# Performance work log

Hardware: AMD Instinct MI355X
Metric: run time of the kernel (lower is better)

The kernel has to match this reference:

```python
import jax, jax.numpy as jnp
import numpy as np

EPS = 1e-6
N_HEADS = 16
KV_HEADS = 4
HEAD_DIM = 64
N_REP = N_HEADS // KV_HEADS
N_EXPERTS = 8
TOP_K = 2


def _rms_norm(x, w):
    return x * jax.lax.rsqrt(jnp.mean(x * x, axis=-1, keepdims=True) + EPS) * w


def _apply_rope(x, fc):
    # x: (B,T,H,D); fc: (T, D//2, 2) holding (cos, sin)
    B, T, H, D = x.shape
    xr = x.reshape(B, T, H, D // 2, 2)
    f = fc.reshape(1, T, 1, D // 2, 2)
    re = xr[..., 0] * f[..., 0] - xr[..., 1] * f[..., 1]
    im = xr[..., 1] * f[..., 0] + xr[..., 0] * f[..., 1]
    return jnp.stack([re, im], axis=-1).reshape(B, T, H, D)


def _silu(x):
    return x * jax.nn.sigmoid(x)


def setup_inputs():
    key = jax.random.key(0)
    ks = jax.random.split(key, 16)
    B, T, C = 4, 1024, 1024
    IE, IS = 1024, 2048  # expert_inter_dim, shared inter_dim
    s = 0.02
    x = jax.random.normal(ks[0], (B, T, C), jnp.float32)
    inv_freq = 1.0 / (10000.0 ** (np.arange(0, HEAD_DIM, 2, dtype=np.float32) / HEAD_DIM))
    ang = np.outer(np.arange(T, dtype=np.float32), inv_freq)
    freq_cis = jnp.asarray(np.stack([np.cos(ang), np.sin(ang)], axis=-1), jnp.float32)
    causal = np.tril(np.ones((T, T), dtype=bool))
    mask = jnp.asarray(np.where(causal, 0.0, -1e9), dtype=jnp.float32).reshape(1, 1, T, T)
    window = jnp.zeros((1, 1, T, T), jnp.float32)
    return {
        "x": x,
        "freq_cis": freq_cis,
        "mask": mask,
        "window": window,
        "norm1_w": jnp.ones((C,), jnp.float32),
        "wq": jax.random.normal(ks[1], (N_HEADS * HEAD_DIM, C), jnp.float32) * s,
        "wk": jax.random.normal(ks[2], (KV_HEADS * HEAD_DIM, C), jnp.float32) * s,
        "wv": jax.random.normal(ks[3], (KV_HEADS * HEAD_DIM, C), jnp.float32) * s,
        "wo": jax.random.normal(ks[4], (C, N_HEADS * HEAD_DIM), jnp.float32) * s,
        "norm2_w": jnp.ones((C,), jnp.float32),
        "gate_w": jax.random.normal(ks[5], (N_EXPERTS, C), jnp.float32) * s,
        "exp_w1": jax.random.normal(ks[6], (N_EXPERTS, IE, C), jnp.float32) * s,
        "exp_w2": jax.random.normal(ks[7], (N_EXPERTS, IE, C), jnp.float32) * s,
        "exp_wp": jax.random.normal(ks[8], (N_EXPERTS, C, IE), jnp.float32) * s,
        "sh_w1": jax.random.normal(ks[9], (IS, C), jnp.float32) * s,
        "sh_w2": jax.random.normal(ks[10], (IS, C), jnp.float32) * s,
        "sh_wp": jax.random.normal(ks[11], (C, IS), jnp.float32) * s,
        "start_pos": 0,
    }


def reference(x, freq_cis, mask, window, norm1_w, wq, wk, wv, wo, norm2_w,
              gate_w, exp_w1, exp_w2, exp_wp, sh_w1, sh_w2, sh_wp, start_pos):
    B, T, C = x.shape
    # ---- pre-norm attention (GQA, Global mask, eval: no dropout) ----
    xn = _rms_norm(x, norm1_w)
    q = (xn @ wq.T).reshape(B, T, N_HEADS, HEAD_DIM)
    k = (xn @ wk.T).reshape(B, T, KV_HEADS, HEAD_DIM)
    v = (xn @ wv.T).reshape(B, T, KV_HEADS, HEAD_DIM)
    q = _apply_rope(q, freq_cis)
    k = _apply_rope(k, freq_cis)
    k = jnp.repeat(k, N_REP, axis=2)  # (B,T,H,D)
    v = jnp.repeat(v, N_REP, axis=2)
    scale = 1.0 / np.sqrt(HEAD_DIM).astype(np.float32)
    att = jnp.einsum("bqhd,bkhd->bhqk", q, k) * scale + mask
    p = jax.nn.softmax(att, axis=-1)
    o = jnp.einsum("bhqk,bkhd->bqhd", p, v).reshape(B, T, C)
    x = x + o @ wo.T
    # ---- pre-norm MoE FFN ----
    xn2 = _rms_norm(x, norm2_w).reshape(-1, C)  # (N,C)
    scores = xn2 @ gate_w.T                      # gate logits, returned
    probs = jax.nn.softmax(scores, axis=-1)
    top_w, top_i = jax.lax.top_k(probs, TOP_K)   # (N,K)
    # dense combine weights (N,E): zero for non-selected experts
    wfull = jnp.sum(jax.nn.one_hot(top_i, N_EXPERTS, dtype=x.dtype) * top_w[..., None], axis=1)
    h = _silu(jnp.einsum("nc,eic->eni", xn2, exp_w1)) * jnp.einsum("nc,eic->eni", xn2, exp_w2)
    ye = jnp.einsum("eni,eci->enc", h, exp_wp)   # per-expert outputs
    y = jnp.einsum("ne,enc->nc", wfull, ye)      # routed combine
    z = (_silu(xn2 @ sh_w1.T) * (xn2 @ sh_w2.T)) @ sh_wp.T  # shared expert
    out = x + (y + z).reshape(B, T, C)
    return out, scores
```

## Files before the change

### kernel.cpp

```cpp
#include <hip/hip_runtime.h>


typedef __bf16 bf16_t;
typedef __bf16 bf16x8 __attribute__((ext_vector_type(8)));
typedef __bf16 bf16x4 __attribute__((ext_vector_type(4)));
typedef float  f32x4  __attribute__((ext_vector_type(4)));

#define LQKV 1536

#define GLD16(gp, lp) __builtin_amdgcn_global_load_lds(                         \
    (const __attribute__((address_space(1))) void*)(gp),                        \
    (__attribute__((address_space(3))) void*)(lp), 16, 0, 0)

#define PIPE_BARRIER() do {                                                     \
    asm volatile("s_waitcnt vmcnt(0)" ::: "memory");                            \
    __builtin_amdgcn_s_barrier();                                               \
} while (0)

__global__ __launch_bounds__(256) void convert_k(
    const float* __restrict__ src, bf16_t* __restrict__ dst)
{
    size_t i = (size_t)blockIdx.x * 256 + threadIdx.x;
    float4 v = *((const float4*)src + i);
    bf16x4 o;
    o[0] = (bf16_t)v.x; o[1] = (bf16_t)v.y; o[2] = (bf16_t)v.z; o[3] = (bf16_t)v.w;
    *((bf16x4*)dst + i) = o;
}

struct Cvt8 {
    const float* s[8];
    bf16_t* d[8];
    int cum[9];
    int nseg;
};

__global__ __launch_bounds__(256) void convert_multi_k(Cvt8 j)
{
    int blk = blockIdx.x;
    int seg = 0;
    while (seg + 1 < j.nseg && blk >= j.cum[seg + 1]) ++seg;
    size_t i = (size_t)(blk - j.cum[seg]) * 256 + threadIdx.x;
    float4 v = *((const float4*)j.s[seg] + i);
    bf16x4 o;
    o[0] = (bf16_t)v.x; o[1] = (bf16_t)v.y; o[2] = (bf16_t)v.z; o[3] = (bf16_t)v.w;
    *((bf16x4*)j.d[seg] + i) = o;
}

__global__ __launch_bounds__(256) void gemm_bt(
    const bf16_t* __restrict__ A, const bf16_t* __restrict__ W,
    int M, int N, int K, int ldw, int mode,
    float* __restrict__ outF, bf16_t* __restrict__ outB,
    const float* __restrict__ resF, float* __restrict__ outF2)
{
    __shared__ __align__(16) bf16_t sA[2][128 * 64];
    __shared__ __align__(16) bf16_t sB[2][128 * 64];
    const int tid  = threadIdx.x;
    const int bm   = blockIdx.y * 128, bn = blockIdx.x * 128;
    const int lane = tid & 63;
    const int wv   = tid >> 6;
    const int wm   = (wv >> 1) * 64, wn = (wv & 1) * 64;
    const int lr   = lane & 15;
    const int kg   = lane >> 4;
    const int swz  = (lr & 7) << 3;

    f32x4 acc[4][4];
    #pragma unroll
    for (int i = 0; i < 4; ++i)
        #pragma unroll
        for (int j = 0; j < 4; ++j)
            acc[i][j] = f32x4{0.f, 0.f, 0.f, 0.f};

    auto STAGE = [&](int b, int k0) {
        #pragma unroll
        for (int p = 0; p < 4; ++p) {
            int idx = p * 256 + tid;
            int row = idx >> 3;
            int ch  = ((idx & 7) * 8) ^ ((row & 7) << 3);
            GLD16(A + (size_t)(bm + row) * K   + k0 + ch, sA[b] + idx * 8);
            GLD16(W + (size_t)(bn + row) * ldw + k0 + ch, sB[b] + idx * 8);
        }
    };

    STAGE(0, 0);
    PIPE_BARRIER();
    int cur = 0;
    for (int k0 = 0; k0 < K; k0 += 64) {
        if (k0 + 64 < K) STAGE(cur ^ 1, k0 + 64);
        #pragma unroll
        for (int ks = 0; ks < 2; ++ks) {
            bf16x8 af[4], bfr[4];
            #pragma unroll
            for (int i = 0; i < 4; ++i)
                af[i] = *(const bf16x8*)(sA[cur] + (wm + i * 16 + lr) * 64 +
                                         ((ks * 32 + kg * 8) ^ swz));
            #pragma unroll
            for (int j = 0; j < 4; ++j)
                bfr[j] = *(const bf16x8*)(sB[cur] + (wn + j * 16 + lr) * 64 +
                                          ((ks * 32 + kg * 8) ^ swz));
            #pragma unroll
            for (int i = 0; i < 4; ++i)
                #pragma unroll
                for (int j = 0; j < 4; ++j)
                    acc[i][j] = __builtin_amdgcn_mfma_f32_16x16x32_bf16(
                        af[i], bfr[j], acc[i][j], 0, 0, 0);
        }
        PIPE_BARRIER();
        cur ^= 1;
    }

    #pragma unroll
    for (int i = 0; i < 4; ++i) {
        #pragma unroll
        for (int j = 0; j < 4; ++j) {
            #pragma unroll
            for (int rr = 0; rr < 4; ++rr) {
                int m = bm + wm + i * 16 + kg * 4 + rr;
                int n = bn + wn + j * 16 + lr;
                size_t o = (size_t)m * N + n;
                float v = acc[i][j][rr];
                if (mode == 0)      outF[o] = v;
                else if (mode == 1) outB[o] = (bf16_t)v;
                else if (mode == 2) {
                    float r = v + resF[o];
                    outF[o] = r;
                    if (outF2) outF2[o] = r;
                } else              outF[o] += v;
            }
        }
    }
}

__global__ __launch_bounds__(256) void gemm_glu(
    const bf16_t* __restrict__ A, const bf16_t* __restrict__ W1,
    const bf16_t* __restrict__ W2, int M, int N, int K,
    bf16_t* __restrict__ out)
{
    __shared__ __align__(16) bf16_t sA[2][128 * 32];
    __shared__ __align__(16) bf16_t sB1[2][128 * 32];
    __shared__ __align__(16) bf16_t sB2[2][128 * 32];
    const int tid  = threadIdx.x;
    const int bm   = blockIdx.y * 128, bn = blockIdx.x * 128;
    const int lane = tid & 63;
    const int wv   = tid >> 6;
    const int wm   = (wv >> 1) * 64, wn = (wv & 1) * 64;
    const int lr   = lane & 15;
    const int kg   = lane >> 4;
    const int rsw  = (lr >> 1) & 3;

    f32x4 acc1[4][4], acc2[4][4];
    #pragma unroll
    for (int i = 0; i < 4; ++i)
        #pragma unroll
        for (int j = 0; j < 4; ++j) {
            acc1[i][j] = f32x4{0.f, 0.f, 0.f, 0.f};
            acc2[i][j] = f32x4{0.f, 0.f, 0.f, 0.f};
        }

    auto STAGE = [&](int b, int k0) {
        #pragma unroll
        for (int p = 0; p < 2; ++p) {
            int idx = p * 256 + tid;
            int row = idx >> 2;
            int ch  = 8 * ((idx & 3) ^ ((idx >> 3) & 3));
            GLD16(A  + (size_t)(bm + row) * K + k0 + ch, sA[b]  + idx * 8);
            GLD16(W1 + (size_t)(bn + row) * K + k0 + ch, sB1[b] + idx * 8);
            GLD16(W2 + (size_t)(bn + row) * K + k0 + ch, sB2[b] + idx * 8);
        }
    };

    STAGE(0, 0);
    PIPE_BARRIER();
    int cur = 0;
    for (int k0 = 0; k0 < K; k0 += 32) {
        if (k0 + 32 < K) STAGE(cur ^ 1, k0 + 32);
        bf16x8 af[4], b1[4], b2[4];
        #pragma unroll
        for (int i = 0; i < 4; ++i)
            af[i] = *(const bf16x8*)(sA[cur] + (wm + i * 16 + lr) * 32 +
                                     8 * (kg ^ rsw));
        #pragma unroll
        for (int j = 0; j < 4; ++j) {
            b1[j] = *(const bf16x8*)(sB1[cur] + (wn + j * 16 + lr) * 32 +
                                     8 * (kg ^ rsw));
            b2[j] = *(const bf16x8*)(sB2[cur] + (wn + j * 16 + lr) * 32 +
                                     8 * (kg ^ rsw));
        }
        #pragma unroll
        for (int i = 0; i < 4; ++i)
            #pragma unroll
            for (int j = 0; j < 4; ++j) {
                acc1[i][j] = __builtin_amdgcn_mfma_f32_16x16x32_bf16(
                    af[i], b1[j], acc1[i][j], 0, 0, 0);
                acc2[i][j] = __builtin_amdgcn_mfma_f32_16x16x32_bf16(
                    af[i], b2[j], acc2[i][j], 0, 0, 0);
            }
        PIPE_BARRIER();
        cur ^= 1;
    }

    #pragma unroll
    for (int i = 0; i < 4; ++i) {
        #pragma unroll
        for (int j = 0; j < 4; ++j) {
            #pragma unroll
            for (int rr = 0; rr < 4; ++rr) {
                int m = bm + wm + i * 16 + kg * 4 + rr;
                int n = bn + wn + j * 16 + lr;
                float v1 = acc1[i][j][rr], v2 = acc2[i][j][rr];
                out[(size_t)m * N + n] = (bf16_t)(v1 / (1.f + __expf(-v1)) * v2);
            }
        }
    }
}

__device__ __forceinline__ int seg_off(const int* cnt, int e)
{
    int r = 0;
    #pragma unroll
    for (int k = 0; k < 8; ++k) if (k < e) r += (cnt[k] + 127) & ~127;
    return r;
}

__global__ __launch_bounds__(256) void glu_gather(
    const bf16_t* __restrict__ A, const bf16_t* __restrict__ W1,
    const bf16_t* __restrict__ W2, const int* __restrict__ tok_list,
    const int* __restrict__ cnt, bf16_t* __restrict__ h)
{
    const int e = blockIdx.y >> 5, t = blockIdx.y & 31;
    const int ce = cnt[e];
    if (t * 128 >= ce) return;
    const int hbase = seg_off(cnt, e) + t * 128;
    const bf16_t* W1e = W1 + (size_t)e * 1048576;
    const bf16_t* W2e = W2 + (size_t)e * 1048576;

    __shared__ __align__(16) bf16_t sA[2][128 * 32];
    __shared__ __align__(16) bf16_t sB1[2][128 * 32];
    __shared__ __align__(16) bf16_t sB2[2][128 * 32];
    const int tid  = threadIdx.x;
    const int bn   = blockIdx.x * 128;
    const int lane = tid & 63;
    const int wv   = tid >> 6;
    const int wm   = (wv >> 1) * 64, wn = (wv & 1) * 64;
    const int lr   = lane & 15;
    const int kg   = lane >> 4;
    const int rsw  = (lr >> 1) & 3;

    int tok2[2];
    #pragma unroll
    for (int p = 0; p < 2; ++p)
        tok2[p] = tok_list[e * 4096 + t * 128 + ((p * 256 + tid) >> 2)];

    f32x4 acc1[4][4], acc2[4][4];
    #pragma unroll
    for (int i = 0; i < 4; ++i)
        #pragma unroll
        for (int j = 0; j < 4; ++j) {
            acc1[i][j] = f32x4{0.f, 0.f, 0.f, 0.f};
            acc2[i][j] = f32x4{0.f, 0.f, 0.f, 0.f};
        }

    auto STAGE = [&](int b, int k0) {
        #pragma unroll
        for (int p = 0; p < 2; ++p) {
            int idx = p * 256 + tid;
            int row = idx >> 2;
            int ch  = 8 * ((idx & 3) ^ ((idx >> 3) & 3));
            GLD16(A   + (size_t)tok2[p] * 1024 + k0 + ch,    sA[b]  + idx * 8);
            GLD16(W1e + (size_t)(bn + row) * 1024 + k0 + ch, sB1[b] + idx * 8);
            GLD16(W2e + (size_t)(bn + row) * 1024 + k0 + ch, sB2[b] + idx * 8);
        }
    };

    STAGE(0, 0);
    PIPE_BARRIER();
    int cur = 0;
    for (int k0 = 0; k0 < 1024; k0 += 32) {
        if (k0 + 32 < 1024) STAGE(cur ^ 1, k0 + 32);
        bf16x8 af[4], b1[4], b2[4];
        #pragma unroll
        for (int i = 0; i < 4; ++i)
            af[i] = *(const bf16x8*)(sA[cur] + (wm + i * 16 + lr) * 32 +
                                     8 * (kg ^ rsw));
        #pragma unroll
        for (int j = 0; j < 4; ++j) {
            b1[j] = *(const bf16x8*)(sB1[cur] + (wn + j * 16 + lr) * 32 +
                                     8 * (kg ^ rsw));
            b2[j] = *(const bf16x8*)(sB2[cur] + (wn + j * 16 + lr) * 32 +
                                     8 * (kg ^ rsw));
        }
        #pragma unroll
        for (int i = 0; i < 4; ++i)
            #pragma unroll
            for (int j = 0; j < 4; ++j) {
                acc1[i][j] = __builtin_amdgcn_mfma_f32_16x16x32_bf16(
                    af[i], b1[j], acc1[i][j], 0, 0, 0);
                acc2[i][j] = __builtin_amdgcn_mfma_f32_16x16x32_bf16(
                    af[i], b2[j], acc2[i][j], 0, 0, 0);
            }
        PIPE_BARRIER();
        cur ^= 1;
    }

    #pragma unroll
    for (int i = 0; i < 4; ++i) {
        #pragma unroll
        for (int j = 0; j < 4; ++j) {
            #pragma unroll
            for (int rr = 0; rr < 4; ++rr) {
                int rl = wm + i * 16 + kg * 4 + rr;
                int n  = bn + wn + j * 16 + lr;
                float v1 = acc1[i][j][rr], v2 = acc2[i][j][rr];
                h[(size_t)(hbase + rl) * 1024 + n] =
                    (bf16_t)(v1 / (1.f + __expf(-v1)) * v2);
            }
        }
    }
}

__global__ __launch_bounds__(256) void down_gather(
    const bf16_t* __restrict__ h, const bf16_t* __restrict__ Wp,
    const int* __restrict__ tok_list, const float* __restrict__ w_list,
    const int* __restrict__ cnt, float* __restrict__ out)
{
    const int e = blockIdx.y >> 5, t = blockIdx.y & 31;
    const int ce = cnt[e];
    if (t * 128 >= ce) return;
    const int hbase = seg_off(cnt, e) + t * 128;
    const bf16_t* We = Wp + (size_t)e * 1048576;

    __shared__ __align__(16) bf16_t sA[2][128 * 64];
    __shared__ __align__(16) bf16_t sB[2][128 * 64];
    const int tid  = threadIdx.x;
    const int bn   = blockIdx.x * 128;
    const int lane = tid & 63;
    const int wv   = tid >> 6;
    const int wm   = (wv >> 1) * 64, wn = (wv & 1) * 64;
    const int lr   = lane & 15;
    const int kg   = lane >> 4;
    const int swz  = (lr & 7) << 3;

    f32x4 acc[4][4];
    #pragma unroll
    for (int i = 0; i < 4; ++i)
        #pragma unroll
        for (int j = 0; j < 4; ++j)
            acc[i][j] = f32x4{0.f, 0.f, 0.f, 0.f};

    auto STAGE = [&](int b, int k0) {
        #pragma unroll
        for (int p = 0; p < 4; ++p) {
            int idx = p * 256 + tid;
            int row = idx >> 3;
            int ch  = ((idx & 7) * 8) ^ ((row & 7) << 3);
            GLD16(h  + (size_t)(hbase + row) * 1024 + k0 + ch, sA[b] + idx * 8);
            GLD16(We + (size_t)(bn + row) * 1024 + k0 + ch,    sB[b] + idx * 8);
        }
    };

    STAGE(0, 0);
    PIPE_BARRIER();
    int cur = 0;
    for (int k0 = 0; k0 < 1024; k0 += 64) {
        if (k0 + 64 < 1024) STAGE(cur ^ 1, k0 + 64);
        #pragma unroll
        for (int ks = 0; ks < 2; ++ks) {
            bf16x8 af[4], bfr[4];
            #pragma unroll
            for (int i = 0; i < 4; ++i)
                af[i] = *(const bf16x8*)(sA[cur] + (wm + i * 16 + lr) * 64 +
                                         ((ks * 32 + kg * 8) ^ swz));
            #pragma unroll
            for (int j = 0; j < 4; ++j)
                bfr[j] = *(const bf16x8*)(sB[cur] + (wn + j * 16 + lr) * 64 +
                                          ((ks * 32 + kg * 8) ^ swz));
            #pragma unroll
            for (int i = 0; i < 4; ++i)
                #pragma unroll
                for (int j = 0; j < 4; ++j)
                    acc[i][j] = __builtin_amdgcn_mfma_f32_16x16x32_bf16(
                        af[i], bfr[j], acc[i][j], 0, 0, 0);
        }
        PIPE_BARRIER();
        cur ^= 1;
    }

    #pragma unroll
    for (int i = 0; i < 4; ++i) {
        #pragma unroll
        for (int rr = 0; rr < 4; ++rr) {
            int g = t * 128 + wm + i * 16 + kg * 4 + rr;
            if (g < ce) {
                int   tok = tok_list[e * 4096 + g];
                float wgt = w_list[e * 4096 + g];
                #pragma unroll
                for (int j = 0; j < 4; ++j) {
                    int n = bn + wn + j * 16 + lr;
                    atomicAdd(&out[(size_t)tok * 1024 + n], wgt * acc[i][j][rr]);
                }
            }
        }
    }
}

__global__ __launch_bounds__(256) void rmsnorm_k(
    const float* __restrict__ src, const float* __restrict__ w,
    bf16_t* __restrict__ dst)
{
    const int row = blockIdx.x, tid = threadIdx.x;
    float4 t4 = *((const float4*)src + (size_t)row * 256 + tid);
    float ssum = t4.x*t4.x + t4.y*t4.y + t4.z*t4.z + t4.w*t4.w;
    #pragma unroll
    for (int off = 32; off > 0; off >>= 1) ssum += __shfl_down(ssum, off);
    __shared__ float red[4];
    if ((tid & 63) == 0) red[tid >> 6] = ssum;
    __syncthreads();
    float total = red[0] + red[1] + red[2] + red[3];
    float rms = rsqrtf(total * (1.0f / 1024.0f) + 1e-6f);
    float4 w4 = *((const float4*)w + tid);
    bf16x4 o4;
    o4[0] = (bf16_t)(t4.x * rms * w4.x);
    o4[1] = (bf16_t)(t4.y * rms * w4.y);
    o4[2] = (bf16_t)(t4.z * rms * w4.z);
    o4[3] = (bf16_t)(t4.w * rms * w4.w);
    *((bf16x4*)dst + (size_t)row * 256 + tid) = o4;
}

__global__ __launch_bounds__(256) void rmsnorm_gate_k(
    const float* __restrict__ src, const float* __restrict__ w,
    const float* __restrict__ gw, bf16_t* __restrict__ dst,
    float* __restrict__ scores, int* __restrict__ topi,
    float* __restrict__ topw)
{
    const int row = blockIdx.x, tid = threadIdx.x;
    float4 t4 = *((const float4*)src + (size_t)row * 256 + tid);
    float ssum = t4.x*t4.x + t4.y*t4.y + t4.z*t4.z + t4.w*t4.w;
    #pragma unroll
    for (int off = 32; off > 0; off >>= 1) ssum += __shfl_down(ssum, off);
    __shared__ float red[4];
    if ((tid & 63) == 0) red[tid >> 6] = ssum;
    __syncthreads();
    float total = red[0] + red[1] + red[2] + red[3];
    float rms = rsqrtf(total * (1.0f / 1024.0f) + 1e-6f);
    float4 w4 = *((const float4*)w + tid);
    float4 f4;
    f4.x = t4.x * rms * w4.x;
    f4.y = t4.y * rms * w4.y;
    f4.z = t4.z * rms * w4.z;
    f4.w = t4.w * rms * w4.w;
    bf16x4 o4;
    o4[0] = (bf16_t)f4.x; o4[1] = (bf16_t)f4.y;
    o4[2] = (bf16_t)f4.z; o4[3] = (bf16_t)f4.w;
    *((bf16x4*)dst + (size_t)row * 256 + tid) = o4;

    float a[8];
    #pragma unroll
    for (int e = 0; e < 8; ++e) {
        float4 g4 = *((const float4*)(gw + (size_t)e * 1024) + tid);
        a[e] = f4.x * g4.x + f4.y * g4.y + f4.z * g4.z + f4.w * g4.w;
    }
    #pragma unroll
    for (int e = 0; e < 8; ++e)
        #pragma unroll
        for (int off = 32; off > 0; off >>= 1) a[e] += __shfl_down(a[e], off);
    __shared__ float gred[4][8];
    if ((tid & 63) == 0)
        #pragma unroll
        for (int e = 0; e < 8; ++e) gred[tid >> 6][e] = a[e];
    __syncthreads();
    if (tid == 0) {
        float lg[8];
        #pragma unroll
        for (int e = 0; e < 8; ++e)
            lg[e] = gred[0][e] + gred[1][e] + gred[2][e] + gred[3][e];
        #pragma unroll
        for (int e = 0; e < 8; ++e) scores[(size_t)row * 8 + e] = lg[e];
        float mx = lg[0];
        #pragma unroll
        for (int e = 1; e < 8; ++e) mx = fmaxf(mx, lg[e]);
        float p[8], sum = 0.f;
        #pragma unroll
        for (int e = 0; e < 8; ++e) { p[e] = __expf(lg[e] - mx); sum += p[e]; }
        float inv = 1.0f / sum;
        #pragma unroll
        for (int e = 0; e < 8; ++e) p[e] *= inv;
        int i1 = 0;
        #pragma unroll
        for (int e = 1; e < 8; ++e) if (p[e] > p[i1]) i1 = e;
        int i2 = (i1 == 0) ? 1 : 0;
        #pragma unroll
        for (int e = 0; e < 8; ++e) if (e != i1 && p[e] > p[i2]) i2 = e;
        topi[row] = i1 | (i2 << 8);
        topw[row * 2]     = p[i1];
        topw[row * 2 + 1] = p[i2];
    }
}

__global__ __launch_bounds__(256) void build_lists_k(
    const int* __restrict__ topi, const float* __restrict__ topw,
    int* __restrict__ tok_list, float* __restrict__ w_list,
    int* __restrict__ cnt)
{
    const int e = blockIdx.x;
    const int tid = threadIdx.x, lane = tid & 63, wv = tid >> 6;
    __shared__ int wc[4];
    int base = 0;
    for (int t0 = 0; t0 < 4096; t0 += 256) {
        int tok = t0 + tid;
        int ti = topi[tok];
        int i1 = ti & 255, i2 = (ti >> 8) & 255;
        bool m = (i1 == e) || (i2 == e);
        unsigned long long b = __ballot(m);
        if (lane == 0) wc[wv] = __popcll(b);
        __syncthreads();
        int pos = base;
        #pragma unroll
        for (int k = 0; k < 4; ++k) if (k < wv) pos += wc[k];
        pos += __popcll(b & ((1ull << lane) - 1ull));
        if (m) {
            tok_list[e * 4096 + pos] = tok;
            w_list[e * 4096 + pos]   = (i1 == e) ? topw[tok * 2] : topw[tok * 2 + 1];
        }
        base += wc[0] + wc[1] + wc[2] + wc[3];
        __syncthreads();
    }
    int padded = (base + 127) & ~127;
    for (int p = base + tid; p < padded; p += 256) tok_list[e * 4096 + p] = 0;
    if (tid == 0) cnt[e] = base;
}

__global__ __launch_bounds__(256) void rope_all_k(
    bf16_t* __restrict__ qkv, const float* __restrict__ fc)
{
    int idx = blockIdx.x * 256 + threadIdx.x;
    int pr = idx & 31;
    int hn = idx >> 5;
    int h  = hn % 20;
    int n  = hn / 20;
    int tpos = n & 1023;
    const float* f = fc + ((size_t)tpos * 32 + pr) * 2;
    float c = f[0], s = f[1];
    int col = (h < 16) ? h * 64 : 1024 + (h - 16) * 64;
    size_t base = (size_t)n * LQKV + col + pr * 2;
    float x0 = (float)qkv[base], x1 = (float)qkv[base + 1];
    qkv[base]     = (bf16_t)(x0 * c - x1 * s);
    qkv[base + 1] = (bf16_t)(x1 * c + x0 * s);
}

__global__ __launch_bounds__(256) void transpose_v(
    const bf16_t* __restrict__ qkv, bf16_t* __restrict__ vt)
{
    __shared__ bf16_t tile[64][72];
    const int tt = blockIdx.x, kvh = blockIdx.y, b = blockIdx.z;
    const int tid = threadIdx.x;
    {
        int r = tid >> 2, c = (tid & 3) * 16;
        const bf16_t* src = qkv + ((size_t)(b * 1024 + tt * 64 + r)) * LQKV
                            + 1280 + kvh * 64 + c;
        bf16x8 v0 = *(const bf16x8*)src;
        bf16x8 v1 = *(const bf16x8*)(src + 8);
        *(bf16x8*)&tile[r][c] = v0;
        *(bf16x8*)&tile[r][c + 8] = v1;
    }
    __syncthreads();
    {
        int d = tid >> 2, t4 = (tid & 3) * 16;
        bf16_t* dst = vt + ((size_t)((b * 4 + kvh) * 64 + d)) * 1024 + tt * 64 + t4;
        bf16x8 o0, o1;
        #pragma unroll
        for (int u = 0; u < 8; ++u) {
            o0[u] = tile[t4 + u][d];
            o1[u] = tile[t4 + 8 + u][d];
        }
        *(bf16x8*)dst = o0;
        *(bf16x8*)(dst + 8) = o1;
    }
}

__global__ __launch_bounds__(256) void attn_mfma(
    const bf16_t* __restrict__ qkv, const bf16_t* __restrict__ vt,
    bf16_t* __restrict__ ob)
{
    const int qt = blockIdx.x, h = blockIdx.y, b = blockIdx.z;
    const int kvh = h >> 2;
    __shared__ __align__(16) bf16_t sK[64 * 64];
    __shared__ __align__(16) bf16_t sVt[64 * 64];
    __shared__ __align__(16) bf16_t sP[64 * 72];
    const int tid  = threadIdx.x;
    const int w    = tid >> 6;
    const int lane = tid & 63;
    const int lr   = lane & 15;
    const int kg   = lane >> 4;
    const int swz  = (lr & 7) << 3;

    bf16x8 qf[2];
    {
        const bf16_t* qrow = qkv + ((size_t)(b * 1024 + qt * 64 + w * 16 + lr)) * LQKV
                             + h * 64;
        qf[0] = *(const bf16x8*)(qrow + kg * 8);
        qf[1] = *(const bf16x8*)(qrow + 32 + kg * 8);
    }
    float m_run[4], l_run[4];
    f32x4 o_acc[4];
    #pragma unroll
    for (int rr = 0; rr < 4; ++rr) { m_run[rr] = -1.0e30f; l_run[rr] = 0.f; }
    #pragma unroll
    for (int dt = 0; dt < 4; ++dt) o_acc[dt] = f32x4{0.f, 0.f, 0.f, 0.f};

    for (int kt = 0; kt <= qt; ++kt) {
        #pragma unroll
        for (int p = 0; p < 2; ++p) {
            int idx = p * 256 + tid;
            int row = idx >> 3;
            int chs = ((idx & 7) * 8) ^ ((row & 7) << 3);
            GLD16(qkv + ((size_t)(b * 1024 + kt * 64 + row)) * LQKV
                      + 1024 + kvh * 64 + chs, sK + idx * 8);
            GLD16(vt + ((size_t)((b * 4 + kvh) * 64 + row)) * 1024 + kt * 64 + chs,
                  sVt + idx * 8);
        }
        __syncthreads();

        f32x4 sfr[4];
        #pragma unroll
        for (int j = 0; j < 4; ++j) {
            sfr[j] = f32x4{0.f, 0.f, 0.f, 0.f};
            #pragma unroll
            for (int ks = 0; ks < 2; ++ks) {
                bf16x8 bf = *(const bf16x8*)(sK + (j * 16 + lr) * 64 +
                                             ((ks * 32 + kg * 8) ^ swz));
                sfr[j] = __builtin_amdgcn_mfma_f32_16x16x32_bf16(qf[ks], bf, sfr[j], 0, 0, 0);
            }
        }
        const int rowg = qt * 64 + w * 16 + kg * 4;
        float mnew[4];
        #pragma unroll
        for (int rr = 0; rr < 4; ++rr) mnew[rr] = m_run[rr];
        #pragma unroll
        for (int j = 0; j < 4; ++j) {
            int colg = kt * 64 + j * 16 + lr;
            #pragma unroll
            for (int rr = 0; rr < 4; ++rr) {
                float s = sfr[j][rr] * 0.125f;
                if (colg > rowg + rr) s = -1.0e30f;
                sfr[j][rr] = s;
                mnew[rr] = fmaxf(mnew[rr], s);
            }
        }
        #pragma unroll
        for (int off = 1; off < 16; off <<= 1)
            #pragma unroll
            for (int rr = 0; rr < 4; ++rr)
                mnew[rr] = fmaxf(mnew[rr], __shfl_xor(mnew[rr], off, 64));
        float alpha[4], lpart[4];
        #pragma unroll
        for (int rr = 0; rr < 4; ++rr) {
            alpha[rr] = __expf(m_run[rr] - mnew[rr]);
            lpart[rr] = 0.f;
        }
        #pragma unroll
        for (int j = 0; j < 4; ++j)
            #pragma unroll
            for (int rr = 0; rr < 4; ++rr) {
                float p = __expf(sfr[j][rr] - mnew[rr]);
                sfr[j][rr] = p;
                lpart[rr] += p;
            }
        #pragma unroll
        for (int j = 0; j < 4; ++j)
            #pragma unroll
            for (int rr = 0; rr < 4; ++rr)
                sP[(w * 16 + kg * 4 + rr) * 72 + j * 16 + lr] = (bf16_t)sfr[j][rr];
        #pragma unroll
        for (int off = 1; off < 16; off <<= 1)
            #pragma unroll
            for (int rr = 0; rr < 4; ++rr)
                lpart[rr] += __shfl_xor(lpart[rr], off, 64);
        #pragma unroll
        for (int rr = 0; rr < 4; ++rr) {
            l_run[rr] = l_run[rr] * alpha[rr] + lpart[rr];
            m_run[rr] = mnew[rr];
        }
        #pragma unroll
        for (int dt = 0; dt < 4; ++dt)
            #pragma unroll
            for (int rr = 0; rr < 4; ++rr)
                o_acc[dt][rr] *= alpha[rr];
        #pragma unroll
        for (int ks = 0; ks < 2; ++ks) {
            bf16x8 af = *(const bf16x8*)(sP + (w * 16 + lr) * 72 + ks * 32 + kg * 8);
            #pragma unroll
            for (int dt = 0; dt < 4; ++dt) {
                bf16x8 bf = *(const bf16x8*)(sVt + (dt * 16 + lr) * 64 +
                                             ((ks * 32 + kg * 8) ^ swz));
                o_acc[dt] = __builtin_amdgcn_mfma_f32_16x16x32_bf16(af, bf, o_acc[dt], 0, 0, 0);
            }
        }
        __syncthreads();
    }

    float inv[4];
    #pragma unroll
    for (int rr = 0; rr < 4; ++rr) inv[rr] = 1.0f / l_run[rr];
    #pragma unroll
    for (int dt = 0; dt < 4; ++dt)
        #pragma unroll
        for (int rr = 0; rr < 4; ++rr) {
            int tok = qt * 64 + w * 16 + kg * 4 + rr;
            ob[((size_t)(b * 1024 + tok)) * 1024 + h * 64 + dt * 16 + lr] =
                (bf16_t)(o_acc[dt][rr] * inv[rr]);
        }
}

extern "C" void kernel_launch(void* const* d_in, const int* in_sizes, int n_in,
                              void* d_out, int out_size, void* d_ws, size_t ws_size,
                              hipStream_t stream)
{
    const float* x   = (const float*)d_in[0];
    const float* fc  = (const float*)d_in[1];
    const float* n1w = (const float*)d_in[4];
    const float* wq  = (const float*)d_in[5];
    const float* wk  = (const float*)d_in[6];
    const float* wv  = (const float*)d_in[7];
    const float* wo  = (const float*)d_in[8];
    const float* n2w = (const float*)d_in[9];
    const float* gw  = (const float*)d_in[10];
    const float* ew1 = (const float*)d_in[11];
    const float* ew2 = (const float*)d_in[12];
    const float* ewp = (const float*)d_in[13];
    const float* sw1 = (const float*)d_in[14];
    const float* sw2 = (const float*)d_in[15];
    const float* swp = (const float*)d_in[16];

    const size_t MB = 1024 * 1024;
    char* ws = (char*)d_ws;
    bf16_t* xnb  = (bf16_t*)(ws + 0);
    float*  x1   = (float*) (ws + 8 * MB);
    bf16_t* ew2b = (bf16_t*)(ws + 8 * MB);
    bf16_t* h    = (bf16_t*)(ws + 24 * MB);
    char*   lists= ws + 42 * MB;
    int*    tok_list = (int*)lists;
    float*  w_list   = (float*)(lists + 131072);
    int*    cnt      = (int*)(lists + 262144);
    int*    topi     = (int*)(lists + 262400);
    float*  topw     = (float*)(lists + 278784);
    bf16_t* sw1b = (bf16_t*)(ws + 43 * MB);
    bf16_t* sw2b = (bf16_t*)(ws + 47 * MB);
    bf16_t* swpb = (bf16_t*)(ws + 51 * MB);
    char*   slotA= ws + 55 * MB;
    bf16_t* hb   = (bf16_t*)slotA;
    bf16_t* qkv  = (bf16_t*)(ws + 71 * MB);
    bf16_t* ob   = (bf16_t*)(ws + 83 * MB);
    bf16_t* vt   = (bf16_t*)(ws + 91 * MB);
    bf16_t* ew1b = (bf16_t*)(ws + 71 * MB);
    bf16_t* ewpb = (bf16_t*)(ws + 71 * MB);

    float* outp   = (float*)d_out;
    float* scores = outp + (size_t)4096 * 1024;

    auto gemm = [&](const bf16_t* A, const bf16_t* W, int M, int N, int K, int ldw,
                    int mode, float* oF, bf16_t* oB, const float* res, float* oF2) {
        gemm_bt<<<dim3(N / 128, M / 128), 256, 0, stream>>>(
            A, W, M, N, K, ldw, mode, oF, oB, res, oF2);
    };

    bf16_t* wqb = (bf16_t*)slotA;
    bf16_t* wkb = wqb + 1048576;
    bf16_t* wvb = wkb + 262144;
    bf16_t* wob = wvb + 262144;
    {
        Cvt8 j;
        j.s[0]=wq;  j.d[0]=wqb;  j.s[1]=wk;  j.d[1]=wkb;
        j.s[2]=wv;  j.d[2]=wvb;  j.s[3]=wo;  j.d[3]=wob;
        j.s[4]=sw1; j.d[4]=sw1b; j.s[5]=sw2; j.d[5]=sw2b;
        j.s[6]=swp; j.d[6]=swpb; j.s[7]=nullptr; j.d[7]=nullptr;
        int sz[7] = {1024, 256, 256, 1024, 2048, 2048, 2048};
        j.cum[0] = 0;
        for (int k = 0; k < 7; ++k) j.cum[k + 1] = j.cum[k] + sz[k];
        j.cum[8] = j.cum[7];
        j.nseg = 7;
        convert_multi_k<<<j.cum[7], 256, 0, stream>>>(j);
    }

    rmsnorm_k<<<4096, 256, 0, stream>>>(x, n1w, xnb);
    gemm(xnb, wqb, 4096, LQKV, 1024, 1024, 1, nullptr, qkv, nullptr, nullptr);
    rope_all_k<<<(4096 * 20 * 32) / 256, 256, 0, stream>>>(qkv, fc);
    transpose_v<<<dim3(16, 4, 4), 256, 0, stream>>>(qkv, vt);
    attn_mfma<<<dim3(16, 16, 4), 256, 0, stream>>>(qkv, vt, ob);
    gemm(ob, wob, 4096, 1024, 1024, 1024, 2, x1, nullptr, x, outp);

    rmsnorm_gate_k<<<4096, 256, 0, stream>>>(x1, n2w, gw, xnb, scores, topi, topw);
    build_lists_k<<<8, 256, 0, stream>>>(topi, topw, tok_list, w_list, cnt);

    {
        Cvt8 j;
        j.s[0]=ew1; j.d[0]=ew1b; j.s[1]=ew2; j.d[1]=ew2b;
        for (int k = 2; k < 8; ++k) { j.s[k]=nullptr; j.d[k]=nullptr; }
        j.cum[0] = 0; j.cum[1] = 8192; j.cum[2] = 16384;
        for (int k = 3; k < 9; ++k) j.cum[k] = 16384;
        j.nseg = 2;
        convert_multi_k<<<16384, 256, 0, stream>>>(j);
    }

    gemm_glu<<<dim3(16, 32), 256, 0, stream>>>(xnb, sw1b, sw2b, 4096, 2048, 1024, hb);
    glu_gather<<<dim3(8, 256), 256, 0, stream>>>(xnb, ew1b, ew2b, tok_list, cnt, h);

    convert_k<<<8192, 256, 0, stream>>>(ewp, ewpb);

    gemm(hb, swpb, 4096, 1024, 2048, 2048, 3, outp, nullptr, nullptr, nullptr);
    down_gather<<<dim3(8, 256), 256, 0, stream>>>(h, ewpb, tok_list, w_list, cnt, outp);

    (void)in_sizes; (void)n_in; (void)out_size; (void)ws_size;
}
```

Before: 635.0 us.

## Switch GEMM kernels to triple-buffered LDS pipeline with partial vmcnt waits

Replaces the double-buffered global-to-LDS pipeline in four GEMM kernels with a three-stage ring buffer that keeps two K-tiles of loads in flight. Each iteration waits only on the oldest tile via a partial vmcnt count, and a second lgkmcnt barrier after compute guards against buffer reuse. gemm_bt and down_gather drop from 64-wide to 32-wide K tiles with a matching swizzle. The aim is to hide global load latency, at the cost of more barriers per unit of K and a heavier LDS footprint in the GLU kernels, which may reduce occupancy.

```diff
diff --git a/kernel.cpp b/kernel.cpp
--- a/kernel.cpp
+++ b/kernel.cpp
@@ -12,8 +12,15 @@
     (const __attribute__((address_space(1))) void*)(gp),                        \
     (__attribute__((address_space(3))) void*)(lp), 16, 0, 0)
 
-#define PIPE_BARRIER() do {                                                     \
-    asm volatile("s_waitcnt vmcnt(0)" ::: "memory");                            \
+#define WAIT_BAR(ahead, L2s, L1s) do {                                          \
+    if ((ahead) == 2)      asm volatile("s_waitcnt vmcnt(" L2s ")" ::: "memory");\
+    else if ((ahead) == 1) asm volatile("s_waitcnt vmcnt(" L1s ")" ::: "memory");\
+    else                   asm volatile("s_waitcnt vmcnt(0)" ::: "memory");     \
+    __builtin_amdgcn_s_barrier();                                               \
+} while (0)
+
+#define BAR_LGKM() do {                                                         \
+    asm volatile("s_waitcnt lgkmcnt(0)" ::: "memory");                          \
     __builtin_amdgcn_s_barrier();                                               \
 } while (0)
 
@@ -52,8 +59,8 @@
     float* __restrict__ outF, bf16_t* __restrict__ outB,
     const float* __restrict__ resF, float* __restrict__ outF2)
 {
-    __shared__ __align__(16) bf16_t sA[2][128 * 64];
-    __shared__ __align__(16) bf16_t sB[2][128 * 64];
+    __shared__ __align__(16) bf16_t sA[3][128 * 32];
+    __shared__ __align__(16) bf16_t sB[3][128 * 32];
     const int tid  = threadIdx.x;
     const int bm   = blockIdx.y * 128, bn = blockIdx.x * 128;
     const int lane = tid & 63;
@@ -61,7 +68,7 @@
     const int wm   = (wv >> 1) * 64, wn = (wv & 1) * 64;
     const int lr   = lane & 15;
     const int kg   = lane >> 4;
-    const int swz  = (lr & 7) << 3;
+    const int rsw  = (lr >> 1) & 3;
 
     f32x4 acc[4][4];
     #pragma unroll
@@ -72,40 +79,40 @@
 
     auto STAGE = [&](int b, int k0) {
         #pragma unroll
-        for (int p = 0; p < 4; ++p) {
+        for (int p = 0; p < 2; ++p) {
             int idx = p * 256 + tid;
-            int row = idx >> 3;
-            int ch  = ((idx & 7) * 8) ^ ((row & 7) << 3);
+            int row = idx >> 2;
+            int ch  = 8 * ((idx & 3) ^ ((idx >> 3) & 3));
             GLD16(A + (size_t)(bm + row) * K   + k0 + ch, sA[b] + idx * 8);
             GLD16(W + (size_t)(bn + row) * ldw + k0 + ch, sB[b] + idx * 8);
         }
     };
 
+    const int T = K >> 5;
     STAGE(0, 0);
-    PIPE_BARRIER();
-    int cur = 0;
-    for (int k0 = 0; k0 < K; k0 += 64) {
-        if (k0 + 64 < K) STAGE(cur ^ 1, k0 + 64);
-        #pragma unroll
-        for (int ks = 0; ks < 2; ++ks) {
-            bf16x8 af[4], bfr[4];
-            #pragma unroll
-            for (int i = 0; i < 4; ++i)
-                af[i] = *(const bf16x8*)(sA[cur] + (wm + i * 16 + lr) * 64 +
-                                         ((ks * 32 + kg * 8) ^ swz));
+    if (T > 1) STAGE(1, 32);
+    int b0 = 0, b1 = 1, b2 = 2;
+    for (int kt = 0; kt < T; ++kt) {
+        if (kt + 2 < T) STAGE(b2, (kt + 2) * 32);
+        int ahead = (kt + 2 < T) ? 2 : ((kt + 1 < T) ? 1 : 0);
+        WAIT_BAR(ahead, "8", "4");
+        const bf16_t* sAr = sA[b0];
+        const bf16_t* sBr = sB[b0];
+        bf16x8 af[4], bfr[4];
+        #pragma unroll
+        for (int i = 0; i < 4; ++i)
+            af[i] = *(const bf16x8*)(sAr + (wm + i * 16 + lr) * 32 + 8 * (kg ^ rsw));
+        #pragma unroll
+        for (int j = 0; j < 4; ++j)
+            bfr[j] = *(const bf16x8*)(sBr + (wn + j * 16 + lr) * 32 + 8 * (kg ^ rsw));
+        #pragma unroll
+        for (int i = 0; i < 4; ++i)
             #pragma unroll
             for (int j = 0; j < 4; ++j)
-                bfr[j] = *(const bf16x8*)(sB[cur] + (wn + j * 16 + lr) * 64 +
-                                          ((ks * 32 + kg * 8) ^ swz));
-            #pragma unroll
-            for (int i = 0; i < 4; ++i)
-                #pragma unroll
-                for (int j = 0; j < 4; ++j)
-                    acc[i][j] = __builtin_amdgcn_mfma_f32_16x16x32_bf16(
-                        af[i], bfr[j], acc[i][j], 0, 0, 0);
-        }
-        PIPE_BARRIER();
-        cur ^= 1;
+                acc[i][j] = __builtin_amdgcn_mfma_f32_16x16x32_bf16(
+                    af[i], bfr[j], acc[i][j], 0, 0, 0);
+        BAR_LGKM();
+        int t = b0; b0 = b1; b1 = b2; b2 = t;
     }
 
     #pragma unroll
@@ -135,9 +142,9 @@
     const bf16_t* __restrict__ W2, int M, int N, int K,
     bf16_t* __restrict__ out)
 {
-    __shared__ __align__(16) bf16_t sA[2][128 * 32];
-    __shared__ __align__(16) bf16_t sB1[2][128 * 32];
-    __shared__ __align__(16) bf16_t sB2[2][128 * 32];
+    __shared__ __align__(16) bf16_t sA[3][128 * 32];
+    __shared__ __align__(16) bf16_t sB1[3][128 * 32];
+    __shared__ __align__(16) bf16_t sB2[3][128 * 32];
     const int tid  = threadIdx.x;
     const int bm   = blockIdx.y * 128, bn = blockIdx.x * 128;
     const int lane = tid & 63;
@@ -168,34 +175,37 @@
         }
     };
 
+    const int T = K >> 5;
     STAGE(0, 0);
-    PIPE_BARRIER();
-    int cur = 0;
-    for (int k0 = 0; k0 < K; k0 += 32) {
-        if (k0 + 32 < K) STAGE(cur ^ 1, k0 + 32);
-        bf16x8 af[4], b1[4], b2[4];
+    if (T > 1) STAGE(1, 32);
+    int b0 = 0, b1 = 1, b2 = 2;
+    for (int kt = 0; kt < T; ++kt) {
+        if (kt + 2 < T) STAGE(b2, (kt + 2) * 32);
+        int ahead = (kt + 2 < T) ? 2 : ((kt + 1 < T) ? 1 : 0);
+        WAIT_BAR(ahead, "12", "6");
+        const bf16_t* sAr  = sA[b0];
+        const bf16_t* sB1r = sB1[b0];
+        const bf16_t* sB2r = sB2[b0];
+        bf16x8 af[4], f1[4], f2[4];
         #pragma unroll
         for (int i = 0; i < 4; ++i)
-            af[i] = *(const bf16x8*)(sA[cur] + (wm + i * 16 + lr) * 32 +
-                                     8 * (kg ^ rsw));
+            af[i] = *(const bf16x8*)(sAr + (wm + i * 16 + lr) * 32 + 8 * (kg ^ rsw));
         #pragma unroll
         for (int j = 0; j < 4; ++j) {
-            b1[j] = *(const bf16x8*)(sB1[cur] + (wn + j * 16 + lr) * 32 +
-                                     8 * (kg ^ rsw));
-            b2[j] = *(const bf16x8*)(sB2[cur] + (wn + j * 16 + lr) * 32 +
-                                     8 * (kg ^ rsw));
+            f1[j] = *(const bf16x8*)(sB1r + (wn + j * 16 + lr) * 32 + 8 * (kg ^ rsw));
+            f2[j] = *(const bf16x8*)(sB2r + (wn + j * 16 + lr) * 32 + 8 * (kg ^ rsw));
         }
         #pragma unroll
         for (int i = 0; i < 4; ++i)
             #pragma unroll
             for (int j = 0; j < 4; ++j) {
                 acc1[i][j] = __builtin_amdgcn_mfma_f32_16x16x32_bf16(
-                    af[i], b1[j], acc1[i][j], 0, 0, 0);
+                    af[i], f1[j], acc1[i][j], 0, 0, 0);
                 acc2[i][j] = __builtin_amdgcn_mfma_f32_16x16x32_bf16(
-                    af[i], b2[j], acc2[i][j], 0, 0, 0);
-            }
-        PIPE_BARRIER();
-        cur ^= 1;
+                    af[i], f2[j], acc2[i][j], 0, 0, 0);
+            }
+        BAR_LGKM();
+        int t = b0; b0 = b1; b1 = b2; b2 = t;
     }
 
     #pragma unroll
@@ -233,9 +243,9 @@
     const bf16_t* W1e = W1 + (size_t)e * 1048576;
     const bf16_t* W2e = W2 + (size_t)e * 1048576;
 
-    __shared__ __align__(16) bf16_t sA[2][128 * 32];
-    __shared__ __align__(16) bf16_t sB1[2][128 * 32];
-    __shared__ __align__(16) bf16_t sB2[2][128 * 32];
+    __shared__ __align__(16) bf16_t sA[3][128 * 32];
+    __shared__ __align__(16) bf16_t sB1[3][128 * 32];
+    __shared__ __align__(16) bf16_t sB2[3][128 * 32];
     const int tid  = threadIdx.x;
     const int bn   = blockIdx.x * 128;
     const int lane = tid & 63;
@@ -272,33 +282,35 @@
     };
 
     STAGE(0, 0);
-    PIPE_BARRIER();
-    int cur = 0;
-    for (int k0 = 0; k0 < 1024; k0 += 32) {
-        if (k0 + 32 < 1024) STAGE(cur ^ 1, k0 + 32);
-        bf16x8 af[4], b1[4], b2[4];
+    STAGE(1, 32);
+    int b0 = 0, b1 = 1, b2 = 2;
+    for (int kt = 0; kt < 32; ++kt) {
+        if (kt + 2 < 32) STAGE(b2, (kt + 2) * 32);
+        int ahead = (kt + 2 < 32) ? 2 : ((kt + 1 < 32) ? 1 : 0);
+        WAIT_BAR(ahead, "12", "6");
+        const bf16_t* sAr  = sA[b0];
+        const bf16_t* sB1r = sB1[b0];
+        const bf16_t* sB2r = sB2[b0];
+        bf16x8 af[4], f1[4], f2[4];
         #pragma unroll
         for (int i = 0; i < 4; ++i)
-            af[i] = *(const bf16x8*)(sA[cur] + (wm + i * 16 + lr) * 32 +
-                                     8 * (kg ^ rsw));
+            af[i] = *(const bf16x8*)(sAr + (wm + i * 16 + lr) * 32 + 8 * (kg ^ rsw));
         #pragma unroll
         for (int j = 0; j < 4; ++j) {
-            b1[j] = *(const bf16x8*)(sB1[cur] + (wn + j * 16 + lr) * 32 +
-                                     8 * (kg ^ rsw));
-            b2[j] = *(const bf16x8*)(sB2[cur] + (wn + j * 16 + lr) * 32 +
-                                     8 * (kg ^ rsw));
+            f1[j] = *(const bf16x8*)(sB1r + (wn + j * 16 + lr) * 32 + 8 * (kg ^ rsw));
+            f2[j] = *(const bf16x8*)(sB2r + (wn + j * 16 + lr) * 32 + 8 * (kg ^ rsw));
         }
         #pragma unroll
         for (int i = 0; i < 4; ++i)
             #pragma unroll
             for (int j = 0; j < 4; ++j) {
                 acc1[i][j] = __builtin_amdgcn_mfma_f32_16x16x32_bf16(
-                    af[i], b1[j], acc1[i][j], 0, 0, 0);
+                    af[i], f1[j], acc1[i][j], 0, 0, 0);
                 acc2[i][j] = __builtin_amdgcn_mfma_f32_16x16x32_bf16(
-                    af[i], b2[j], acc2[i][j], 0, 0, 0);
-            }
-        PIPE_BARRIER();
-        cur ^= 1;
+                    af[i], f2[j], acc2[i][j], 0, 0, 0);
+            }
+        BAR_LGKM();
+        int tt = b0; b0 = b1; b1 = b2; b2 = tt;
     }
 
     #pragma unroll
@@ -328,8 +340,8 @@
     const int hbase = seg_off(cnt, e) + t * 128;
     const bf16_t* We = Wp + (size_t)e * 1048576;
 
-    __shared__ __align__(16) bf16_t sA[2][128 * 64];
-    __shared__ __align__(16) bf16_t sB[2][128 * 64];
+    __shared__ __align__(16) bf16_t sA[3][128 * 32];
+    __shared__ __align__(16) bf16_t sB[3][128 * 32];
     const int tid  = threadIdx.x;
     const int bn   = blockIdx.x * 128;
     const int lane = tid & 63;
@@ -337,7 +349,7 @@
     const int wm   = (wv >> 1) * 64, wn = (wv & 1) * 64;
     const int lr   = lane & 15;
     const int kg   = lane >> 4;
-    const int swz  = (lr & 7) << 3;
+    const int rsw  = (lr >> 1) & 3;
 
     f32x4 acc[4][4];
     #pragma unroll
@@ -348,40 +360,39 @@
 
     auto STAGE = [&](int b, int k0) {
         #pragma unroll
-        for (int p = 0; p < 4; ++p) {
+        for (int p = 0; p < 2; ++p) {
             int idx = p * 256 + tid;
-            int row = idx >> 3;
-            int ch  = ((idx & 7) * 8) ^ ((row & 7) << 3);
+            int row = idx >> 2;
+            int ch  = 8 * ((idx & 3) ^ ((idx >> 3) & 3));
             GLD16(h  + (size_t)(hbase + row) * 1024 + k0 + ch, sA[b] + idx * 8);
             GLD16(We + (size_t)(bn + row) * 1024 + k0 + ch,    sB[b] + idx * 8);
         }
     };
 
     STAGE(0, 0);
-    PIPE_BARRIER();
-    int cur = 0;
-    for (int k0 = 0; k0 < 1024; k0 += 64) {
-        if (k0 + 64 < 1024) STAGE(cur ^ 1, k0 + 64);
-        #pragma unroll
-        for (int ks = 0; ks < 2; ++ks) {
-            bf16x8 af[4], bfr[4];
-            #pragma unroll
-            for (int i = 0; i < 4; ++i)
-                af[i] = *(const bf16x8*)(sA[cur] + (wm + i * 16 + lr) * 64 +
-                                         ((ks * 32 + kg * 8) ^ swz));
+    STAGE(1, 32);
+    int b0 = 0, b1 = 1, b2 = 2;
+    for (int kt = 0; kt < 32; ++kt) {
+        if (kt + 2 < 32) STAGE(b2, (kt + 2) * 32);
+        int ahead = (kt + 2 < 32) ? 2 : ((kt + 1 < 32) ? 1 : 0);
+        WAIT_BAR(ahead, "8", "4");
+        const bf16_t* sAr = sA[b0];
+        const bf16_t* sBr = sB[b0];
+        bf16x8 af[4], bfr[4];
+        #pragma unroll
+        for (int i = 0; i < 4; ++i)
+            af[i] = *(const bf16x8*)(sAr + (wm + i * 16 + lr) * 32 + 8 * (kg ^ rsw));
+        #pragma unroll
+        for (int j = 0; j < 4; ++j)
+            bfr[j] = *(const bf16x8*)(sBr + (wn + j * 16 + lr) * 32 + 8 * (kg ^ rsw));
+        #pragma unroll
+        for (int i = 0; i < 4; ++i)
             #pragma unroll
             for (int j = 0; j < 4; ++j)
-                bfr[j] = *(const bf16x8*)(sB[cur] + (wn + j * 16 + lr) * 64 +
-                                          ((ks * 32 + kg * 8) ^ swz));
-            #pragma unroll
-            for (int i = 0; i < 4; ++i)
-                #pragma unroll
-                for (int j = 0; j < 4; ++j)
-                    acc[i][j] = __builtin_amdgcn_mfma_f32_16x16x32_bf16(
-                        af[i], bfr[j], acc[i][j], 0, 0, 0);
-        }
-        PIPE_BARRIER();
-        cur ^= 1;
+                acc[i][j] = __builtin_amdgcn_mfma_f32_16x16x32_bf16(
+                    af[i], bfr[j], acc[i][j], 0, 0, 0);
+        BAR_LGKM();
+        int tt = b0; b0 = b1; b1 = b2; b2 = tt;
     }
 
     #pragma unroll
```

After: 638.6 us. Within noise of the previous version (+0.6%).
